# Kernel tuning notes

Measured on AMD Instinct MI355X. Metric: run time of the kernel, lower is better.

Reference implementation:

```python
import jax, jax.numpy as jnp
import numpy as np
from itertools import product

_N = 50000
_G = 52  # voxel grid extent


def _build_maps():
    rs = np.random.RandomState(0)
    ids = rs.choice(_G ** 3, size=_N, replace=False)
    coords = np.stack(np.unravel_index(ids, (_G, _G, _G)), axis=1)  # [N,3]
    order = np.argsort(ids)
    sorted_ids = ids[order]
    in_lists, out_lists = [], []
    for off in product((-1, 0, 1), repeat=3):
        nb = coords + np.array(off)
        valid = np.all((nb >= 0) & (nb < _G), axis=1)
        nb_id = nb[:, 0] * _G * _G + nb[:, 1] * _G + nb[:, 2]
        pos = np.searchsorted(sorted_ids, nb_id)
        pos_c = np.minimum(pos, _N - 1)
        found = valid & (sorted_ids[pos_c] == nb_id)
        in_lists.append(order[pos_c[found]].astype(np.int32))
        out_lists.append(np.nonzero(found)[0].astype(np.int32))
    P = max(len(a) for a in in_lists)  # identity offset -> P == N
    K = len(in_lists)
    in_idx = np.full((K, P), _N, dtype=np.int32)   # sentinel = zero row
    out_idx = np.full((K, P), _N, dtype=np.int32)  # sentinel = dummy out row
    for k in range(K):
        in_idx[k, : len(in_lists[k])] = in_lists[k]
        out_idx[k, : len(out_lists[k])] = out_lists[k]
    pid = (coords[:, 0] // 2) * 26 * 26 + (coords[:, 1] // 2) * 26 + (coords[:, 2] // 2)
    uniq, inv = np.unique(pid, return_inverse=True)
    return in_idx, out_idx, inv.astype(np.int32), int(len(uniq))


def setup_inputs() -> dict:
    key = jax.random.key(0)
    ks = jax.random.split(key, 10)
    in_idx, out_idx, pool_idx, num_pool = _build_maps()
    s1 = 1.0 / np.sqrt(27 * 256)
    s2 = 1.0 / np.sqrt(27 * 512)
    return {
        "feats": jax.random.normal(ks[0], (_N, 256), jnp.float32),
        "W1": jax.random.normal(ks[1], (27, 256, 512), jnp.float32) * s1,
        "g1": 1.0 + 0.1 * jax.random.normal(ks[2], (512,), jnp.float32),
        "b1": 0.05 * jax.random.normal(ks[3], (512,), jnp.float32),
        "W2": jax.random.normal(ks[4], (27, 512, 512), jnp.float32) * s2,
        "g2": 1.0 + 0.1 * jax.random.normal(ks[5], (512,), jnp.float32),
        "b2": 0.05 * jax.random.normal(ks[6], (512,), jnp.float32),
        "W3": jax.random.normal(ks[7], (27, 512, 512), jnp.float32) * s2,
        "g3": 1.0 + 0.1 * jax.random.normal(ks[8], (512,), jnp.float32),
        "b3": 0.05 * jax.random.normal(ks[9], (512,), jnp.float32),
        "in_idx": jnp.asarray(in_idx),
        "out_idx": jnp.asarray(out_idx),
        "pool_idx": jnp.asarray(pool_idx),
        "num_pool": num_pool,
    }


def _sparse_conv(feats, W, in_idx, out_idx):
    # gather-GEMM-scatter over K=27 kernel offsets (MinkowskiConvolution)
    N, Cin = feats.shape
    fp = jnp.concatenate([feats, jnp.zeros((1, Cin), feats.dtype)], axis=0)
    acc0 = jnp.zeros((N + 1, W.shape[-1]), feats.dtype)  # last row = dummy sink
    def step(acc, xs):
        ii, oi, Wk = xs
        return acc.at[oi].add(fp[ii] @ Wk), None
    acc, _ = jax.lax.scan(step, acc0, (in_idx, out_idx, W))
    return acc[:N]


def _bn_relu(x, g, b, eps=1e-5):
    m = x.mean(axis=0)
    v = x.var(axis=0)  # biased, matching torch BN normalization
    return jax.nn.relu((x - m) * jax.lax.rsqrt(v + eps) * g + b)


def reference(feats, W1, g1, b1, W2, g2, b2, W3, g3, b3, in_idx, out_idx, pool_idx, num_pool):
    x = _bn_relu(_sparse_conv(feats, W1, in_idx, out_idx), g1, b1)
    x = _bn_relu(_sparse_conv(x, W2, in_idx, out_idx), g2, b2)
    x = _bn_relu(_sparse_conv(x, W3, in_idx, out_idx), g3, b3)
    return jax.ops.segment_max(x, pool_idx, num_segments=num_pool)
```

## Files before the change

### kernel.cpp

```cpp
#include <hip/hip_runtime.h>
#include <hip/hip_bf16.h>
#include <stdint.h>

typedef __attribute__((ext_vector_type(8))) short bf16x8;
typedef __attribute__((ext_vector_type(4))) float f32x4;
typedef unsigned short u16;

__device__ __forceinline__ u16 f2bf(float x) {
  unsigned u = __float_as_uint(x);
  unsigned r = (u + 0x7FFFu + ((u >> 16) & 1u)) >> 16;
  return (u16)r;
}

__device__ __forceinline__ void gl_lds16(const void* g, void* l) {
  __builtin_amdgcn_global_load_lds((const __attribute__((address_space(1))) void*)g,
                                   (__attribute__((address_space(3))) void*)l, 16, 0, 0);
}


__global__ void zero_i32_kernel(int* p, int n) {
  int i = blockIdx.x * blockDim.x + threadIdx.x;
  if (i < n) p[i] = 0;
}

__global__ void init_nbr_kernel(int* nbr, int total, int N) {
  for (int i = blockIdx.x * blockDim.x + threadIdx.x; i < total; i += gridDim.x * blockDim.x)
    nbr[i] = N;
}

__global__ void scatter_nbr_kernel(const int* __restrict__ in_idx, const int* __restrict__ out_idx,
                                   int* __restrict__ nbr, int N, int P, int NPAD) {
  const int total = 27 * P;
  for (int i = blockIdx.x * blockDim.x + threadIdx.x; i < total; i += gridDim.x * blockDim.x) {
    const int o = out_idx[i];
    if ((unsigned)o < (unsigned)N) {
      const int k = i / P;
      nbr[(size_t)k * NPAD + o] = in_idx[i];
    }
  }
}

__global__ void cvt_feats_kernel(const float* __restrict__ F, u16* __restrict__ X0, int N) {
  const int total = (N + 1) * 64;
  for (int i = blockIdx.x * blockDim.x + threadIdx.x; i < total; i += gridDim.x * blockDim.x) {
    const int r = i >> 6;
    ushort4 o;
    if (r < N) {
      const float4 v = ((const float4*)F)[i];
      o.x = f2bf(v.x); o.y = f2bf(v.y); o.z = f2bf(v.z); o.w = f2bf(v.w);
    } else {
      o.x = 0; o.y = 0; o.z = 0; o.w = 0;
    }
    ((ushort4*)X0)[i] = o;
  }
}

__global__ void cvt_w_kernel(const float* __restrict__ W, u16* __restrict__ Wt, int CIN) {
  __shared__ float t[32][33];
  const int k = blockIdx.z;
  const int c0 = blockIdx.y * 32;
  const int n0 = blockIdx.x * 32;
  const int tx = threadIdx.x, ty = threadIdx.y;
  const float* Wk = W + (size_t)k * CIN * 512;
  for (int i = ty; i < 32; i += 8)
    t[i][tx] = Wk[(size_t)(c0 + i) * 512 + n0 + tx];
  __syncthreads();
  u16* Wtk = Wt + (size_t)k * 512 * CIN;
  for (int i = ty; i < 32; i += 8)
    Wtk[(size_t)(n0 + i) * CIN + c0 + tx] = f2bf(t[tx][i]);
}


__global__ void scatter_members_kernel(const int* __restrict__ pool_idx, int* __restrict__ gcnt,
                                       int* __restrict__ mlist, int N) {
  const int r = blockIdx.x * blockDim.x + threadIdx.x;
  if (r < N) {
    const int p = pool_idx[r];
    const int pos = atomicAdd(&gcnt[p], 1);
    if (pos < 8) mlist[p * 8 + pos] = r;
  }
}

__global__ void pool_grouped_kernel(const float* __restrict__ Y, const float* __restrict__ sc,
                                    const float* __restrict__ sh, const int* __restrict__ gcnt,
                                    const int* __restrict__ mlist, float* __restrict__ out) {
  const int p = blockIdx.x;
  const int t = threadIdx.x;
  const int c = t * 2;
  const float s0 = sc[c], s1 = sc[c + 1];
  const float h0 = sh[c], h1 = sh[c + 1];
  int n = gcnt[p];
  if (n > 8) n = 8;
  float m0 = 0.f, m1 = 0.f;
  for (int i = 0; i < n; ++i) {
    const int r = mlist[p * 8 + i];
    const float2 v = *(const float2*)&Y[(size_t)r * 512 + c];
    m0 = fmaxf(m0, fmaxf(fmaf(v.x, s0, h0), 0.f));
    m1 = fmaxf(m1, fmaxf(fmaf(v.y, s1, h1), 0.f));
  }
  float2 o; o.x = m0; o.y = m1;
  *(float2*)&out[(size_t)p * 512 + c] = o;
}


template <int CIN>
__global__ __launch_bounds__(256, 2) void conv_kernel(
    const u16* __restrict__ X,
    const u16* __restrict__ Wt,
    const int* __restrict__ nbr,
    float* __restrict__ Y,
    float* __restrict__ st,
    int N, int NPAD) {
  constexpr int KK = CIN / 32;
  __shared__ __align__(16) u16 lds[24576];

  const int tid = threadIdx.x;
  const int lane = tid & 63;
  const int wv = tid >> 6;
  const int wm = wv >> 1, wn = wv & 1;

  int bid = blockIdx.x;
  if ((gridDim.x & 7) == 0) {
    const int cpx = gridDim.x >> 3;
    bid = (bid & 7) * cpx + (bid >> 3);
  }
  const int row0 = (bid >> 2) * 128;
  const int col0 = (bid & 3) * 128;

  const int srow = tid >> 2;
  const int scs = (((tid & 3) ^ ((srow >> 1) & 3)) * 8);
  const size_t boffg0 = (size_t)(col0 + srow) * CIN + scs;
  const size_t boffg1 = (size_t)(col0 + 64 + srow) * CIN + scs;

  const int lr = lane & 15;
  const int q = lane >> 4;
  int aoff[4], boff[4];
#pragma unroll
  for (int f = 0; f < 4; ++f) {
    const int ra = wm * 64 + f * 16 + lr;
    aoff[f] = ra * 32 + ((q ^ ((ra >> 1) & 3)) * 8);
    const int rb = wn * 64 + f * 16 + lr;
    boff[f] = 4096 + rb * 32 + ((q ^ ((rb >> 1) & 3)) * 8);
  }

  f32x4 acc[4][4];
#pragma unroll
  for (int a = 0; a < 4; ++a)
#pragma unroll
    for (int b = 0; b < 4; ++b) acc[a][b] = (f32x4){0.f, 0.f, 0.f, 0.f};

  auto stage = [&](int slot, size_t a0, size_t a1, int ko, size_t kb) {
    u16* sb = &lds[slot * 8192];
    gl_lds16(X + a0 + ko + scs, &sb[wv * 512]);
    gl_lds16(X + a1 + ko + scs, &sb[2048 + wv * 512]);
    gl_lds16(Wt + kb + boffg0 + ko, &sb[4096 + wv * 512]);
    gl_lds16(Wt + kb + boffg1 + ko, &sb[6144 + wv * 512]);
  };

  size_t arow0 = (size_t)nbr[row0 + srow] * CIN;
  size_t arow1 = (size_t)nbr[row0 + 64 + srow] * CIN;
  stage(0, arow0, arow1, 0, 0);
  stage(1, arow0, arow1, 32, 0);

  int sl = 0, sl2 = 2;
  int nn0 = 0, nn1 = 0;

#define STEP_BODY(WAITN, DO_NBR, DO_STAGE, A0, A1, KO, KB)                        \
  {                                                                               \
    asm volatile("s_waitcnt vmcnt(" #WAITN ")" ::: "memory");                     \
    __builtin_amdgcn_s_barrier();                                                 \
    asm volatile("" ::: "memory");                                                \
    const u16* lb = &lds[sl * 8192];                                              \
    bf16x8 av[4], bv[4];                                                          \
    _Pragma("unroll") for (int f = 0; f < 4; ++f) av[f] = *(const bf16x8*)&lb[aoff[f]]; \
    _Pragma("unroll") for (int f = 0; f < 4; ++f) bv[f] = *(const bf16x8*)&lb[boff[f]]; \
    __builtin_amdgcn_sched_barrier(0);                                            \
    if (DO_NBR) {                                                                 \
      nn0 = nbr[(size_t)(s + 1) * NPAD + row0 + srow];                            \
      nn1 = nbr[(size_t)(s + 1) * NPAD + row0 + 64 + srow];                       \
    }                                                                             \
    if (DO_STAGE) stage(sl2, (A0), (A1), (KO), (KB));                             \
    __builtin_amdgcn_sched_barrier(0);                                            \
    __builtin_amdgcn_s_setprio(1);                                                \
    _Pragma("unroll") for (int a = 0; a < 4; ++a)                                 \
      _Pragma("unroll") for (int b = 0; b < 4; ++b)                               \
        acc[a][b] = __builtin_amdgcn_mfma_f32_16x16x32_bf16(av[a], bv[b], acc[a][b], 0, 0, 0); \
    __builtin_amdgcn_s_setprio(0);                                                \
    sl = (sl == 2) ? 0 : sl + 1;                                                  \
    sl2 = (sl2 == 2) ? 0 : sl2 + 1;                                               \
  }

  for (int s = 0; s < 26; ++s) {
    const size_t kbC = (size_t)s * (512 * CIN);
    const size_t kbN = (size_t)(s + 1) * (512 * CIN);
#pragma unroll
    for (int kk = 0; kk < KK; ++kk) {
      const bool donbr = (kk == 2);
      if (kk < KK - 2) {
        if (kk == 3) STEP_BODY(6, donbr, true, arow0, arow1, (kk + 2) * 32, kbC)
        else         STEP_BODY(4, donbr, true, arow0, arow1, (kk + 2) * 32, kbC)
      } else {
        STEP_BODY(4, false, true, (size_t)nn0 * CIN, (size_t)nn1 * CIN,
                  (kk + 2 - KK) * 32, kbN)
      }
    }
    arow0 = (size_t)nn0 * CIN;
    arow1 = (size_t)nn1 * CIN;
  }
  {
    const int s = 26;
    const size_t kbC = (size_t)s * (512 * CIN);
    (void)s;
#pragma unroll
    for (int kk = 0; kk < KK; ++kk) {
      if (kk < KK - 2)      STEP_BODY(4, false, true, arow0, arow1, (kk + 2) * 32, kbC)
      else if (kk < KK - 1) STEP_BODY(4, false, false, arow0, arow1, 0, kbC)
      else                  STEP_BODY(0, false, false, arow0, arow1, 0, kbC)
    }
  }
#undef STEP_BODY

#pragma unroll
  for (int a = 0; a < 4; ++a) {
    const int r0 = row0 + wm * 64 + a * 16 + q * 4;
#pragma unroll
    for (int b = 0; b < 4; ++b) {
      const int c = col0 + wn * 64 + b * 16 + lr;
#pragma unroll
      for (int j = 0; j < 4; ++j) {
        const int r = r0 + j;
        if (r < N) Y[(size_t)r * 512 + c] = acc[a][b][j];
      }
    }
  }

  __syncthreads();
  float* fls = (float*)lds;
  if (tid < 256) fls[tid] = 0.f;
  __syncthreads();
#pragma unroll
  for (int b = 0; b < 4; ++b) {
    float s = 0.f, q2 = 0.f;
#pragma unroll
    for (int a = 0; a < 4; ++a) {
      const int rbase = row0 + wm * 64 + a * 16 + q * 4;
#pragma unroll
      for (int j = 0; j < 4; ++j) {
        if (rbase + j < N) {
          const float v = acc[a][b][j];
          s += v; q2 += v * v;
        }
      }
    }
    s += __shfl_xor(s, 16);  s += __shfl_xor(s, 32);
    q2 += __shfl_xor(q2, 16); q2 += __shfl_xor(q2, 32);
    if (q == 0) {
      const int cl = wn * 64 + b * 16 + lr;
      atomicAdd(&fls[cl], s);
      atomicAdd(&fls[128 + cl], q2);
    }
  }
  __syncthreads();
  if (tid < 128) {
    atomicAdd(&st[col0 + tid], fls[tid]);
    atomicAdd(&st[512 + col0 + tid], fls[128 + tid]);
  }
}


__global__ void bn_finalize_kernel(const float* __restrict__ st, const float* __restrict__ g,
                                   const float* __restrict__ b, float* __restrict__ sc,
                                   float* __restrict__ sh, int N) {
  const int c = threadIdx.x;
  if (c < 512) {
    const float inv = 1.f / (float)N;
    const float m = st[c] * inv;
    const float v = st[512 + c] * inv - m * m;
    const float rs = rsqrtf(v + 1e-5f);
    const float s = rs * g[c];
    sc[c] = s;
    sh[c] = b[c] - m * s;
  }
}

__global__ void bn_norm_kernel(const float* __restrict__ Y, const float* __restrict__ sc,
                               const float* __restrict__ sh, u16* __restrict__ Xn, int N) {
  const int total = (N + 1) * 128;
  for (int i = blockIdx.x * blockDim.x + threadIdx.x; i < total; i += gridDim.x * blockDim.x) {
    const int r = i >> 7;
    const int c = (i & 127) * 4;
    ushort4 o;
    if (r < N) {
      const float4 y = *(const float4*)&Y[(size_t)r * 512 + c];
      const float v0 = fmaxf(fmaf(y.x, sc[c + 0], sh[c + 0]), 0.f);
      const float v1 = fmaxf(fmaf(y.y, sc[c + 1], sh[c + 1]), 0.f);
      const float v2 = fmaxf(fmaf(y.z, sc[c + 2], sh[c + 2]), 0.f);
      const float v3 = fmaxf(fmaf(y.w, sc[c + 3], sh[c + 3]), 0.f);
      o.x = f2bf(v0); o.y = f2bf(v1); o.z = f2bf(v2); o.w = f2bf(v3);
    } else {
      o.x = 0; o.y = 0; o.z = 0; o.w = 0;
    }
    *(ushort4*)&Xn[(size_t)r * 512 + c] = o;
  }
}


extern "C" void kernel_launch(void* const* d_in, const int* in_sizes, int n_in,
                              void* d_out, int out_size, void* d_ws, size_t ws_size,
                              hipStream_t stream) {
  const float* feats = (const float*)d_in[0];
  const float* W1 = (const float*)d_in[1];
  const float* g1 = (const float*)d_in[2];
  const float* b1 = (const float*)d_in[3];
  const float* W2 = (const float*)d_in[4];
  const float* g2 = (const float*)d_in[5];
  const float* b2 = (const float*)d_in[6];
  const float* W3 = (const float*)d_in[7];
  const float* g3 = (const float*)d_in[8];
  const float* b3 = (const float*)d_in[9];
  const int* in_idx = (const int*)d_in[10];
  const int* out_idx = (const int*)d_in[11];
  const int* pool_idx = (const int*)d_in[12];
  float* out = (float*)d_out;

  const int N = in_sizes[0] / 256;
  const int P = in_sizes[10] / 27;
  const int NPAD = ((N + 127) / 128) * 128;
  const int npool = out_size / 512;
  (void)n_in; (void)ws_size;

  char* w = (char*)d_ws;
  size_t off = 0;
  auto carve = [&](size_t bytes) {
    void* p = w + off;
    off += (bytes + 511) & ~(size_t)511;
    return p;
  };
  u16* X0 = (u16*)carve((size_t)(N + 1) * 256 * 2);
  u16* X1 = (u16*)carve((size_t)(N + 1) * 512 * 2);
  float* Y = (float*)carve((size_t)N * 512 * 4);
  u16* W1t = (u16*)carve((size_t)27 * 512 * 256 * 2);
  u16* W2t = (u16*)carve((size_t)27 * 512 * 512 * 2);
  u16* W3t = (u16*)carve((size_t)27 * 512 * 512 * 2);
  float* st0 = (float*)carve(1024 * 4);
  float* st1 = (float*)carve(1024 * 4);
  float* st2 = (float*)carve(1024 * 4);
  float* sc = (float*)carve(512 * 4);
  float* sh = (float*)carve(512 * 4);
  int* nbr = (int*)carve((size_t)27 * NPAD * 4);

  int* gcnt = (int*)X0;
  int* mlist = (int*)((char*)X0 + (1 << 17));

  const int convGrid = (NPAD / 128) * 4;

  zero_i32_kernel<<<4, 256, 0, stream>>>((int*)st0, 1024);
  zero_i32_kernel<<<4, 256, 0, stream>>>((int*)st1, 1024);
  zero_i32_kernel<<<4, 256, 0, stream>>>((int*)st2, 1024);
  init_nbr_kernel<<<2048, 256, 0, stream>>>(nbr, 27 * NPAD, N);
  scatter_nbr_kernel<<<2048, 256, 0, stream>>>(in_idx, out_idx, nbr, N, P, NPAD);
  cvt_feats_kernel<<<2048, 256, 0, stream>>>(feats, X0, N);
  cvt_w_kernel<<<dim3(16, 8, 27), dim3(32, 8), 0, stream>>>(W1, W1t, 256);
  cvt_w_kernel<<<dim3(16, 16, 27), dim3(32, 8), 0, stream>>>(W2, W2t, 512);
  cvt_w_kernel<<<dim3(16, 16, 27), dim3(32, 8), 0, stream>>>(W3, W3t, 512);

  conv_kernel<256><<<convGrid, 256, 0, stream>>>(X0, W1t, nbr, Y, st0, N, NPAD);
  zero_i32_kernel<<<(npool + 255) / 256, 256, 0, stream>>>(gcnt, npool);
  scatter_members_kernel<<<(N + 255) / 256, 256, 0, stream>>>(pool_idx, gcnt, mlist, N);
  bn_finalize_kernel<<<1, 512, 0, stream>>>(st0, g1, b1, sc, sh, N);
  bn_norm_kernel<<<4096, 256, 0, stream>>>(Y, sc, sh, X1, N);

  conv_kernel<512><<<convGrid, 256, 0, stream>>>(X1, W2t, nbr, Y, st1, N, NPAD);
  bn_finalize_kernel<<<1, 512, 0, stream>>>(st1, g2, b2, sc, sh, N);
  bn_norm_kernel<<<4096, 256, 0, stream>>>(Y, sc, sh, X1, N);

  conv_kernel<512><<<convGrid, 256, 0, stream>>>(X1, W3t, nbr, Y, st2, N, NPAD);
  bn_finalize_kernel<<<1, 512, 0, stream>>>(st2, g3, b3, sc, sh, N);
  pool_grouped_kernel<<<npool, 256, 0, stream>>>(Y, sc, sh, gcnt, mlist, out);
}
```

Measured before the change: 1.778 ms.

## Load weight fragments directly into registers, halve LDS, raise occupancy to three

```diff
diff --git a/kernel.cpp b/kernel.cpp
--- a/kernel.cpp
+++ b/kernel.cpp
@@ -104,7 +104,7 @@
 
 
 template <int CIN>
-__global__ __launch_bounds__(256, 2) void conv_kernel(
+__global__ __launch_bounds__(256, 3) void conv_kernel(
     const u16* __restrict__ X,
     const u16* __restrict__ Wt,
     const int* __restrict__ nbr,
@@ -112,7 +112,7 @@
     float* __restrict__ st,
     int N, int NPAD) {
   constexpr int KK = CIN / 32;
-  __shared__ __align__(16) u16 lds[24576];
+  __shared__ __align__(16) u16 lds[12288];
 
   const int tid = threadIdx.x;
   const int lane = tid & 63;
@@ -129,19 +129,19 @@
 
   const int srow = tid >> 2;
   const int scs = (((tid & 3) ^ ((srow >> 1) & 3)) * 8);
-  const size_t boffg0 = (size_t)(col0 + srow) * CIN + scs;
-  const size_t boffg1 = (size_t)(col0 + 64 + srow) * CIN + scs;
 
   const int lr = lane & 15;
   const int q = lane >> 4;
-  int aoff[4], boff[4];
+  int aoff[4];
 #pragma unroll
   for (int f = 0; f < 4; ++f) {
     const int ra = wm * 64 + f * 16 + lr;
     aoff[f] = ra * 32 + ((q ^ ((ra >> 1) & 3)) * 8);
-    const int rb = wn * 64 + f * 16 + lr;
-    boff[f] = 4096 + rb * 32 + ((q ^ ((rb >> 1) & 3)) * 8);
-  }
+  }
+  size_t bfrag[4];
+#pragma unroll
+  for (int f = 0; f < 4; ++f)
+    bfrag[f] = (size_t)(col0 + wn * 64 + f * 16 + lr) * CIN + q * 8;
 
   f32x4 acc[4][4];
 #pragma unroll
@@ -149,45 +149,57 @@
 #pragma unroll
     for (int b = 0; b < 4; ++b) acc[a][b] = (f32x4){0.f, 0.f, 0.f, 0.f};
 
-  auto stage = [&](int slot, size_t a0, size_t a1, int ko, size_t kb) {
-    u16* sb = &lds[slot * 8192];
+  auto stageA = [&](int slot, size_t a0, size_t a1, int ko) {
+    u16* sb = &lds[slot * 4096];
     gl_lds16(X + a0 + ko + scs, &sb[wv * 512]);
     gl_lds16(X + a1 + ko + scs, &sb[2048 + wv * 512]);
-    gl_lds16(Wt + kb + boffg0 + ko, &sb[4096 + wv * 512]);
-    gl_lds16(Wt + kb + boffg1 + ko, &sb[6144 + wv * 512]);
   };
 
   size_t arow0 = (size_t)nbr[row0 + srow] * CIN;
   size_t arow1 = (size_t)nbr[row0 + 64 + srow] * CIN;
-  stage(0, arow0, arow1, 0, 0);
-  stage(1, arow0, arow1, 32, 0);
+
+  bf16x8 bv0[4], bv1[4], av[4];
+
+  stageA(0, arow0, arow1, 0);
+  __builtin_amdgcn_sched_barrier(0);
+#pragma unroll
+  for (int f = 0; f < 4; ++f) bv0[f] = *(const bf16x8*)(Wt + bfrag[f]);
+  __builtin_amdgcn_sched_barrier(0);
+  stageA(1, arow0, arow1, 32);
+  __builtin_amdgcn_sched_barrier(0);
+#pragma unroll
+  for (int f = 0; f < 4; ++f) bv1[f] = *(const bf16x8*)(Wt + 32 + bfrag[f]);
+  __builtin_amdgcn_sched_barrier(0);
 
   int sl = 0, sl2 = 2;
   int nn0 = 0, nn1 = 0;
 
-#define STEP_BODY(WAITN, DO_NBR, DO_STAGE, A0, A1, KO, KB)                        \
-  {                                                                               \
-    asm volatile("s_waitcnt vmcnt(" #WAITN ")" ::: "memory");                     \
-    __builtin_amdgcn_s_barrier();                                                 \
-    asm volatile("" ::: "memory");                                                \
-    const u16* lb = &lds[sl * 8192];                                              \
-    bf16x8 av[4], bv[4];                                                          \
+#define STEP(WAITN, DO_NBR, DO_STAGE, A0, A1, KO2, KB2, BV)                         \
+  {                                                                                 \
+    asm volatile("s_waitcnt vmcnt(" #WAITN ")" ::: "memory");                       \
+    __builtin_amdgcn_s_barrier();                                                   \
+    asm volatile("" ::: "memory");                                                  \
+    const u16* lb = &lds[sl * 4096];                                                \
     _Pragma("unroll") for (int f = 0; f < 4; ++f) av[f] = *(const bf16x8*)&lb[aoff[f]]; \
-    _Pragma("unroll") for (int f = 0; f < 4; ++f) bv[f] = *(const bf16x8*)&lb[boff[f]]; \
-    __builtin_amdgcn_sched_barrier(0);                                            \
-    if (DO_NBR) {                                                                 \
-      nn0 = nbr[(size_t)(s + 1) * NPAD + row0 + srow];                            \
-      nn1 = nbr[(size_t)(s + 1) * NPAD + row0 + 64 + srow];                       \
-    }                                                                             \
-    if (DO_STAGE) stage(sl2, (A0), (A1), (KO), (KB));                             \
-    __builtin_amdgcn_sched_barrier(0);                                            \
-    __builtin_amdgcn_s_setprio(1);                                                \
-    _Pragma("unroll") for (int a = 0; a < 4; ++a)                                 \
-      _Pragma("unroll") for (int b = 0; b < 4; ++b)                               \
-        acc[a][b] = __builtin_amdgcn_mfma_f32_16x16x32_bf16(av[a], bv[b], acc[a][b], 0, 0, 0); \
-    __builtin_amdgcn_s_setprio(0);                                                \
-    sl = (sl == 2) ? 0 : sl + 1;                                                  \
-    sl2 = (sl2 == 2) ? 0 : sl2 + 1;                                               \
+    __builtin_amdgcn_sched_barrier(0);                                              \
+    if (DO_NBR) {                                                                   \
+      nn0 = nbr[(size_t)(s + 1) * NPAD + row0 + srow];                              \
+      nn1 = nbr[(size_t)(s + 1) * NPAD + row0 + 64 + srow];                         \
+    }                                                                               \
+    if (DO_STAGE) stageA(sl2, (A0), (A1), (KO2));                                   \
+    __builtin_amdgcn_sched_barrier(0);                                              \
+    __builtin_amdgcn_s_setprio(1);                                                  \
+    _Pragma("unroll") for (int a = 0; a < 4; ++a)                                   \
+      _Pragma("unroll") for (int b = 0; b < 4; ++b)                                 \
+        acc[a][b] = __builtin_amdgcn_mfma_f32_16x16x32_bf16(av[a], BV[b], acc[a][b], 0, 0, 0); \
+    __builtin_amdgcn_s_setprio(0);                                                  \
+    if (DO_STAGE) {                                                                 \
+      const u16* bp = Wt + (KB2) + (KO2);                                           \
+      _Pragma("unroll") for (int f = 0; f < 4; ++f) BV[f] = *(const bf16x8*)(bp + bfrag[f]); \
+    }                                                                               \
+    __builtin_amdgcn_sched_barrier(0);                                              \
+    sl = (sl == 2) ? 0 : sl + 1;                                                    \
+    sl2 = (sl2 == 2) ? 0 : sl2 + 1;                                                 \
   }
 
   for (int s = 0; s < 26; ++s) {
@@ -195,13 +207,16 @@
     const size_t kbN = (size_t)(s + 1) * (512 * CIN);
 #pragma unroll
     for (int kk = 0; kk < KK; ++kk) {
-      const bool donbr = (kk == 2);
-      if (kk < KK - 2) {
-        if (kk == 3) STEP_BODY(6, donbr, true, arow0, arow1, (kk + 2) * 32, kbC)
-        else         STEP_BODY(4, donbr, true, arow0, arow1, (kk + 2) * 32, kbC)
+      if ((kk & 1) == 0) {
+        if (kk == 2)        STEP(6, true, true, arow0, arow1, (kk + 2) * 32, kbC, bv0)
+        else if (kk < KK - 2) STEP(6, false, true, arow0, arow1, (kk + 2) * 32, kbC, bv0)
+        else                STEP(6, false, true, (size_t)nn0 * CIN, (size_t)nn1 * CIN,
+                                 (kk + 2 - KK) * 32, kbN, bv0)
       } else {
-        STEP_BODY(4, false, true, (size_t)nn0 * CIN, (size_t)nn1 * CIN,
-                  (kk + 2 - KK) * 32, kbN)
+        if (kk == 3)        STEP(8, false, true, arow0, arow1, (kk + 2) * 32, kbC, bv1)
+        else if (kk < KK - 2) STEP(6, false, true, arow0, arow1, (kk + 2) * 32, kbC, bv1)
+        else                STEP(6, false, true, (size_t)nn0 * CIN, (size_t)nn1 * CIN,
+                                 (kk + 2 - KK) * 32, kbN, bv1)
       }
     }
     arow0 = (size_t)nn0 * CIN;
@@ -213,12 +228,16 @@
     (void)s;
 #pragma unroll
     for (int kk = 0; kk < KK; ++kk) {
-      if (kk < KK - 2)      STEP_BODY(4, false, true, arow0, arow1, (kk + 2) * 32, kbC)
-      else if (kk < KK - 1) STEP_BODY(4, false, false, arow0, arow1, 0, kbC)
-      else                  STEP_BODY(0, false, false, arow0, arow1, 0, kbC)
-    }
-  }
-#undef STEP_BODY
+      if ((kk & 1) == 0) {
+        if (kk < KK - 2) STEP(6, false, true, arow0, arow1, (kk + 2) * 32, kbC, bv0)
+        else             STEP(6, false, false, arow0, arow1, 0, kbC, bv0)
+      } else {
+        if (kk < KK - 2) STEP(6, false, true, arow0, arow1, (kk + 2) * 32, kbC, bv1)
+        else             STEP(0, false, false, arow0, arow1, 0, kbC, bv1)
+      }
+    }
+  }
+#undef STEP
 
 #pragma unroll
   for (int a = 0; a < 4; ++a) {
```

Measured after the change: 4.000 ms. +125.0%, slower.
